# Performance work log

Hardware: AMD Instinct MI355X
Metric: run time of the kernel (lower is better)

The kernel has to match this reference:

```python
import jax, jax.numpy as jnp
import numpy as np

B, L, T = 256, 1024, 128

def setup_inputs() -> dict:
    key = jax.random.key(0)
    k1, k2, k3, k4 = jax.random.split(key, 4)
    inputs = jax.random.normal(k1, (B, L, T), dtype=jnp.float32)
    tag_indices = jax.random.randint(k2, (B, L), 0, T, dtype=jnp.int64)
    sequence_lengths = jax.random.randint(k3, (B,), 1, L + 1, dtype=jnp.int64)
    # xavier-ish scale for transitions
    transition_params = jax.random.normal(k4, (T, T), dtype=jnp.float32) * (2.0 / (T + T)) ** 0.5
    return {"inputs": inputs, "tag_indices": tag_indices,
            "sequence_lengths": sequence_lengths, "transition_params": transition_params}

def _crf_log_likelihood(inputs, tag_indices, sequence_lengths, transition_params):
    b, l, t = inputs.shape
    mask = (jnp.arange(l)[None, :] < sequence_lengths[:, None]).astype(inputs.dtype)  # [B,L]

    # --- unary score: sum_t inputs[b, t, tag[b,t]] over valid t ---
    unary = jnp.take_along_axis(inputs, tag_indices[:, :, None], axis=2)[:, :, 0]  # [B,L]
    unary_score = jnp.sum(unary * mask, axis=1)

    # --- binary score: sum_t trans[tag[t], tag[t+1]] masked by mask[:,1:] ---
    trans_sc = transition_params[tag_indices[:, :-1], tag_indices[:, 1:]]  # [B,L-1]
    binary_score = jnp.sum(trans_sc * mask[:, 1:], axis=1)
    sequence_scores = unary_score + binary_score

    # --- log normalizer via forward algorithm (log-space scan) ---
    first = inputs[:, 0]                               # [B,T]
    rest = jnp.transpose(inputs[:, 1:], (1, 0, 2))     # [L-1,B,T]

    def step(state, inp_t):
        # state: [B,T] previous alphas; transition broadcast: [B,T_prev,T_next]
        new = inp_t + jax.nn.logsumexp(state[:, :, None] + transition_params[None], axis=1)
        return new, new

    _, alphas = jax.lax.scan(step, first, rest)        # [L-1,B,T]
    # original indexes all_alphas at max(0, seq_len - 2)
    idx = jnp.clip(sequence_lengths - 2, 0, l - 2)
    final_alphas = alphas[idx, jnp.arange(b)]          # [B,T]
    log_norm = jax.nn.logsumexp(final_alphas, axis=1)
    log_norm = jnp.where(sequence_lengths <= 0, jnp.zeros_like(log_norm), log_norm)

    return sequence_scores - log_norm

def reference(inputs, tag_indices, sequence_lengths, transition_params):
    return _crf_log_likelihood(inputs, tag_indices, sequence_lengths, transition_params)
```

## Files before the change

kernel.cpp:

```cpp
#include <hip/hip_runtime.h>


#define B_   256
#define LL   1024
#define TT   128
#define NBLK 16
#define L2E  1.4426950408889634f
#define LN2f 0.6931471805599453f

typedef __attribute__((ext_vector_type(8))) short bf16x8;
typedef __attribute__((ext_vector_type(4))) float f32x4;
union bfrw { unsigned w[4]; bf16x8 v; };

__device__ __forceinline__ unsigned bfround(float x) {
    unsigned u = __float_as_uint(x);
    return u + 0x7fffu + ((u >> 16) & 1u);
}
__device__ __forceinline__ void lds_barrier() {
    asm volatile("s_waitcnt lgkmcnt(0)\n\ts_barrier" ::: "memory");
}

__global__ void crf_score(const float* __restrict__ inputs,
                          const int*   __restrict__ tags,
                          const int*   __restrict__ slens,
                          const float* __restrict__ trans,
                          float* __restrict__ scorebuf) {
    const int b = blockIdx.x, tid = threadIdx.x;
    const int lane = tid & 63, wid = tid >> 6;
    __shared__ float wsc[4];
    const int slen = slens[b];
    const float* inb  = inputs + (size_t)b * LL * TT;
    const int*   tagb = tags + b * LL;
    float sc = 0.f;
    for (int t = tid; t < slen; t += 256) {
        int tg = tagb[t];
        float v = inb[(size_t)t * TT + tg];
        if (t >= 1) v += trans[tagb[t - 1] * TT + tg];
        sc += v;
    }
    #pragma unroll
    for (int off = 32; off > 0; off >>= 1) sc += __shfl_xor(sc, off, 64);
    if (lane == 0) wsc[wid] = sc;
    __syncthreads();
    if (tid == 0) scorebuf[b] = wsc[0] + wsc[1] + wsc[2] + wsc[3];
}

template<bool FWD, int PH>
__device__ __forceinline__ void phase(int t, float& Dacc, float4 (&up)[4][2],
                                      const bf16x8 (&af)[2][4],
                                      short* qls, float* sb, const float* pu,
                                      float* __restrict__ qcap, float* __restrict__ rcap,
                                      float* __restrict__ dqv, float* __restrict__ drv,
                                      int cb, int tfin, int rank,
                                      int wid, int quad, int bl)
{
    constexpr int CUR  = PH & 1;
    constexpr int NXT  = CUR ^ 1;
    constexpr int SLOT = FWD ? ((1 + PH) & 3) : ((3 - PH) & 3);

    bfrw bfr[4];
    #pragma unroll
    for (int c = 0; c < 4; ++c)
        bfr[c].v = *(const bf16x8*)(qls + CUR * (16 * 136) + bl * 136 + (4 * c + quad) * 8);
    float sprev = sb[CUR * 16 + bl];

    float ex[8];
    #pragma unroll
    for (int mt = 0; mt < 2; ++mt) {
        float4 v = up[SLOT][mt];
        ex[4*mt+0] = __builtin_amdgcn_exp2f(v.x * L2E);
        ex[4*mt+1] = __builtin_amdgcn_exp2f(v.y * L2E);
        ex[4*mt+2] = __builtin_amdgcn_exp2f(v.z * L2E);
        ex[4*mt+3] = __builtin_amdgcn_exp2f(v.w * L2E);
    }
    {
        int tp = FWD ? (t + 4) : (t - 5);
        tp = tp < 0 ? 0 : (tp > LL - 1 ? LL - 1 : tp);
        #pragma unroll
        for (int mt = 0; mt < 2; ++mt)
            up[SLOT][mt] = *(const float4*)(pu + (size_t)tp * TT + mt * 16);
    }

    f32x4 a0 = {0.f,0.f,0.f,0.f}, a1 = {0.f,0.f,0.f,0.f};
    #pragma unroll
    for (int c = 0; c < 4; ++c) {
        a0 = __builtin_amdgcn_mfma_f32_16x16x32_bf16(af[0][c], bfr[c].v, a0, 0, 0, 0);
        a1 = __builtin_amdgcn_mfma_f32_16x16x32_bf16(af[1][c], bfr[c].v, a1, 0, 0, 0);
    }

    float ci = __builtin_amdgcn_rcpf(sprev);
    Dacc += __builtin_amdgcn_logf(sprev);
    float rv[8];
    #pragma unroll
    for (int r = 0; r < 4; ++r) { rv[r] = ci * a0[r]; rv[4 + r] = ci * a1[r]; }

    if (!FWD) {
        bool cap = (cb == t - 1);
        if (__any(cap)) {
            if (cap) {
                float4 s0 = {rv[0], rv[1], rv[2], rv[3]};
                float4 s1 = {rv[4], rv[5], rv[6], rv[7]};
                *(float4*)(rcap + rank * TT + wid * 32 + quad * 4) = s0;
                *(float4*)(rcap + rank * TT + wid * 32 + 16 + quad * 4) = s1;
                if (wid == 0 && quad == 0) drv[rank] = Dacc;
            }
        }
        bool inj = (tfin == t - 1);
        #pragma unroll
        for (int k = 0; k < 8; ++k) rv[k] = inj ? 1.0f : rv[k];
        Dacc = inj ? 0.0f : Dacc;
    }

    float ov[8];
    #pragma unroll
    for (int k = 0; k < 8; ++k) ov[k] = ex[k] * rv[k];

    if (FWD) {
        bool cap = (cb == t);
        if (__any(cap)) {
            if (cap) {
                float4 s0 = {ov[0], ov[1], ov[2], ov[3]};
                float4 s1 = {ov[4], ov[5], ov[6], ov[7]};
                *(float4*)(qcap + rank * TT + wid * 32 + quad * 4) = s0;
                *(float4*)(qcap + rank * TT + wid * 32 + 16 + quad * 4) = s1;
                if (wid == 0 && quad == 0) dqv[rank] = Dacc;
            }
        }
    }

    if (wid == 0 && quad == 0) sb[NXT * 16 + bl] = a0[0];

    bfrw pk;
    pk.w[0] = __builtin_amdgcn_perm(bfround(ov[1]), bfround(ov[0]), 0x07060302);
    pk.w[1] = __builtin_amdgcn_perm(bfround(ov[3]), bfround(ov[2]), 0x07060302);
    pk.w[2] = __builtin_amdgcn_perm(bfround(ov[5]), bfround(ov[4]), 0x07060302);
    pk.w[3] = __builtin_amdgcn_perm(bfround(ov[7]), bfround(ov[6]), 0x07060302);
    *(bf16x8*)(qls + NXT * (16 * 136) + bl * 136 + (4 * wid + quad) * 8) = pk.v;

    lds_barrier();
}

__launch_bounds__(256, 1)
__global__ void crf_scan(const float* __restrict__ inputs,
                         const int*   __restrict__ slens,
                         const float* __restrict__ trans,
                         float* __restrict__ qcap, float* __restrict__ rcap,
                         float* __restrict__ dqv,  float* __restrict__ drv,
                         int* __restrict__ perm)
{
    __shared__ __align__(16) short qls[2 * 16 * 136];
    __shared__ float sb[2 * 16];
    __shared__ int keys[B_];

    const int tid  = threadIdx.x;
    const int lane = tid & 63;
    const int wid  = __builtin_amdgcn_readfirstlane(tid >> 6);
    const int quad = lane >> 4;
    const int bl   = lane & 15;
    const bool isf = (blockIdx.x < NBLK);
    const int g    = isf ? blockIdx.x : blockIdx.x - NBLK;

    keys[tid] = slens[tid] * 256 + tid;
    __syncthreads();
    for (int k = 2; k <= B_; k <<= 1) {
        for (int s = k >> 1; s > 0; s >>= 1) {
            int ixj = tid ^ s;
            if (ixj > tid) {
                int a = keys[tid], b2 = keys[ixj];
                bool asc = ((tid & k) == 0);
                if ((a > b2) == asc) { keys[tid] = b2; keys[ixj] = a; }
            }
            __syncthreads();
        }
    }
    if (isf && tid < 16) perm[g * 16 + tid] = keys[g * 16 + tid] & 255;

    const int key = keys[g * 16 + bl];
    const int ob  = key & 255;
    const int sl  = key >> 8;
    int tfin = sl - 1; if (tfin < 1) tfin = 1;
    const int cb = tfin >> 1;

    int cmax = cb, cmin = cb, tmax = tfin;
    #pragma unroll
    for (int o = 1; o < 16; o <<= 1) {
        int a = __shfl_xor(cmax, o, 16); cmax = a > cmax ? a : cmax;
        int b2 = __shfl_xor(cmin, o, 16); cmin = b2 < cmin ? b2 : cmin;
        int c2 = __shfl_xor(tmax, o, 16); tmax = c2 > tmax ? c2 : tmax;
    }
    cmax = __builtin_amdgcn_readfirstlane(cmax);
    cmin = __builtin_amdgcn_readfirstlane(cmin);
    tmax = __builtin_amdgcn_readfirstlane(tmax);

    bf16x8 af[2][4];
    #pragma unroll
    for (int mt = 0; mt < 2; ++mt) {
        const int j = wid * 32 + mt * 16 + bl;
        #pragma unroll
        for (int c = 0; c < 4; ++c) {
            #pragma unroll
            for (int jj = 0; jj < 8; ++jj) {
                int k = 32 * c + 16 * (jj >> 2) + 4 * quad + (jj & 3);
                int idx = isf ? (k * TT + j) : (j * TT + k);
                float ev = __builtin_amdgcn_exp2f(trans[idx] * L2E);
                af[mt][c][jj] = (short)(bfround(ev) >> 16);
            }
        }
    }

    const float* pu = inputs + (size_t)ob * LL * TT + wid * 32 + quad * 4;
    const int rank = g * 16 + bl;
    float Dacc = 0.f;
    float4 up[4][2];

    if (tid < 16) sb[tid] = 1.0f;

    if (isf) {
        float q0[8];
        #pragma unroll
        for (int mt = 0; mt < 2; ++mt) {
            float4 v = *(const float4*)(pu + mt * 16);
            q0[4*mt+0] = __builtin_amdgcn_exp2f(v.x * L2E);
            q0[4*mt+1] = __builtin_amdgcn_exp2f(v.y * L2E);
            q0[4*mt+2] = __builtin_amdgcn_exp2f(v.z * L2E);
            q0[4*mt+3] = __builtin_amdgcn_exp2f(v.w * L2E);
        }
        bfrw pk;
        pk.w[0] = __builtin_amdgcn_perm(bfround(q0[1]), bfround(q0[0]), 0x07060302);
        pk.w[1] = __builtin_amdgcn_perm(bfround(q0[3]), bfround(q0[2]), 0x07060302);
        pk.w[2] = __builtin_amdgcn_perm(bfround(q0[5]), bfround(q0[4]), 0x07060302);
        pk.w[3] = __builtin_amdgcn_perm(bfround(q0[7]), bfround(q0[6]), 0x07060302);
        *(bf16x8*)(qls + bl * 136 + (4 * wid + quad) * 8) = pk.v;
        if (cb == 0) {
            float4 s0 = {q0[0], q0[1], q0[2], q0[3]};
            float4 s1 = {q0[4], q0[5], q0[6], q0[7]};
            *(float4*)(qcap + rank * TT + wid * 32 + quad * 4) = s0;
            *(float4*)(qcap + rank * TT + wid * 32 + 16 + quad * 4) = s1;
            if (wid == 0 && quad == 0) dqv[rank] = 0.f;
        }
        #pragma unroll
        for (int s = 1; s <= 4; ++s) {
            #pragma unroll
            for (int mt = 0; mt < 2; ++mt)
                up[s & 3][mt] = *(const float4*)(pu + (size_t)s * TT + mt * 16);
        }
        __syncthreads();

        for (int tb = 1; tb <= cmax; tb += 4) {
            phase<true,0>(tb+0, Dacc, up, af, qls, sb, pu, qcap, rcap, dqv, drv, cb, tfin, rank, wid, quad, bl);
            phase<true,1>(tb+1, Dacc, up, af, qls, sb, pu, qcap, rcap, dqv, drv, cb, tfin, rank, wid, quad, bl);
            phase<true,2>(tb+2, Dacc, up, af, qls, sb, pu, qcap, rcap, dqv, drv, cb, tfin, rank, wid, quad, bl);
            phase<true,3>(tb+3, Dacc, up, af, qls, sb, pu, qcap, rcap, dqv, drv, cb, tfin, rank, wid, quad, bl);
        }
    } else {
        bfrw pk;
        pk.w[0] = pk.w[1] = pk.w[2] = pk.w[3] = 0x3F803F80u;
        *(bf16x8*)(qls + bl * 136 + (4 * wid + quad) * 8) = pk.v;

        const int tb0 = (tmax + 4) & ~3;
        #pragma unroll
        for (int ph = 0; ph < 4; ++ph) {
            int ui = tb0 - 1 - ph;
            ui = ui > LL - 1 ? LL - 1 : (ui < 0 ? 0 : ui);
            #pragma unroll
            for (int mt = 0; mt < 2; ++mt)
                up[(3 - ph) & 3][mt] = *(const float4*)(pu + (size_t)ui * TT + mt * 16);
        }
        __syncthreads();

        for (int tb = tb0; tb > cmin; tb -= 4) {
            phase<false,0>(tb-0, Dacc, up, af, qls, sb, pu, qcap, rcap, dqv, drv, cb, tfin, rank, wid, quad, bl);
            phase<false,1>(tb-1, Dacc, up, af, qls, sb, pu, qcap, rcap, dqv, drv, cb, tfin, rank, wid, quad, bl);
            phase<false,2>(tb-2, Dacc, up, af, qls, sb, pu, qcap, rcap, dqv, drv, cb, tfin, rank, wid, quad, bl);
            phase<false,3>(tb-3, Dacc, up, af, qls, sb, pu, qcap, rcap, dqv, drv, cb, tfin, rank, wid, quad, bl);
        }
    }
}

__global__ void crf_comb(const float* __restrict__ qcap, const float* __restrict__ rcap,
                         const float* __restrict__ dqv, const float* __restrict__ drv,
                         const int* __restrict__ perm, const float* __restrict__ scorebuf,
                         float* __restrict__ out) {
    const int tid = threadIdx.x;
    const int r16 = tid >> 4, part = tid & 15;
    const int rank = blockIdx.x * 16 + r16;
    const float* qc = qcap + rank * TT + part * 8;
    const float* rc = rcap + rank * TT + part * 8;
    float4 a0 = *(const float4*)(qc);
    float4 a1 = *(const float4*)(qc + 4);
    float4 b0 = *(const float4*)(rc);
    float4 b1 = *(const float4*)(rc + 4);
    float s = a0.x*b0.x + a0.y*b0.y + a0.z*b0.z + a0.w*b0.w
            + a1.x*b1.x + a1.y*b1.y + a1.z*b1.z + a1.w*b1.w;
    #pragma unroll
    for (int o = 1; o < 16; o <<= 1) s += __shfl_xor(s, o, 16);
    if (part == 0) {
        int ob = perm[rank];
        float logZ = LN2f * (__builtin_amdgcn_logf(s) + dqv[rank] + drv[rank]);
        out[ob] = scorebuf[ob] - logZ;
    }
}

extern "C" void kernel_launch(void* const* d_in, const int* in_sizes, int n_in,
                              void* d_out, int out_size, void* d_ws, size_t ws_size,
                              hipStream_t stream) {
    const float* inputs = (const float*)d_in[0];
    const int*   tags   = (const int*)d_in[1];
    const int*   slens  = (const int*)d_in[2];
    const float* trans  = (const float*)d_in[3];
    float* out = (float*)d_out;

    float* qcap = (float*)d_ws;
    float* rcap = qcap + 32768;
    float* dqv  = rcap + 32768;
    float* drv  = dqv + 256;
    int*   perm = (int*)(drv + 256);
    float* scorebuf = (float*)(perm + 256);

    crf_score<<<B_, 256, 0, stream>>>(inputs, tags, slens, trans, scorebuf);
    crf_scan<<<2 * NBLK, 256, 0, stream>>>(inputs, slens, trans, qcap, rcap, dqv, drv, perm);
    crf_comb<<<NBLK, 256, 0, stream>>>(qcap, rcap, dqv, drv, perm, scorebuf, out);
}
```

Before: 430.7 us.

## Fuse score kernel into scan launch, rebalance meet-in-middle split, split MFMA chains

Moves the gold-path score computation into 64 extra blocks of the scan kernel, removing one launch and letting it run alongside the 32 scan blocks. The forward/backward meeting point becomes the group-wide midpoint of the longest sequence in each group rather than each sequence's own half, which balances the forward and backward blocks. The four chained MFMAs are split into two independent accumulator chains to shorten the dependency chain, and bf16 packing uses a hardware convert builtin when available. Risks: the extra blocks contend with the scan blocks for memory bandwidth, and the new capture logic for sequences whose meeting point equals their final step must stay correct.

```diff
diff --git a/kernel.cpp b/kernel.cpp
--- a/kernel.cpp
+++ b/kernel.cpp
@@ -16,33 +16,16 @@
     unsigned u = __float_as_uint(x);
     return u + 0x7fffu + ((u >> 16) & 1u);
 }
+__device__ __forceinline__ unsigned pack2(float lo, float hi) {
+#if __has_builtin(__builtin_amdgcn_cvt_pk_bf16_f32)
+    auto p = __builtin_amdgcn_cvt_pk_bf16_f32(lo, hi);
+    unsigned w; __builtin_memcpy(&w, &p, 4); return w;
+#else
+    return __builtin_amdgcn_perm(bfround(hi), bfround(lo), 0x07060302);
+#endif
+}
 __device__ __forceinline__ void lds_barrier() {
     asm volatile("s_waitcnt lgkmcnt(0)\n\ts_barrier" ::: "memory");
-}
-
-__global__ void crf_score(const float* __restrict__ inputs,
-                          const int*   __restrict__ tags,
-                          const int*   __restrict__ slens,
-                          const float* __restrict__ trans,
-                          float* __restrict__ scorebuf) {
-    const int b = blockIdx.x, tid = threadIdx.x;
-    const int lane = tid & 63, wid = tid >> 6;
-    __shared__ float wsc[4];
-    const int slen = slens[b];
-    const float* inb  = inputs + (size_t)b * LL * TT;
-    const int*   tagb = tags + b * LL;
-    float sc = 0.f;
-    for (int t = tid; t < slen; t += 256) {
-        int tg = tagb[t];
-        float v = inb[(size_t)t * TT + tg];
-        if (t >= 1) v += trans[tagb[t - 1] * TT + tg];
-        sc += v;
-    }
-    #pragma unroll
-    for (int off = 32; off > 0; off >>= 1) sc += __shfl_xor(sc, off, 64);
-    if (lane == 0) wsc[wid] = sc;
-    __syncthreads();
-    if (tid == 0) scorebuf[b] = wsc[0] + wsc[1] + wsc[2] + wsc[3];
 }
 
 template<bool FWD, int PH>
@@ -63,6 +46,18 @@
     for (int c = 0; c < 4; ++c)
         bfr[c].v = *(const bf16x8*)(qls + CUR * (16 * 136) + bl * 136 + (4 * c + quad) * 8);
     float sprev = sb[CUR * 16 + bl];
+    float ci = __builtin_amdgcn_rcpf(sprev);
+
+    f32x4 ae0 = {0.f,0.f,0.f,0.f}, ao0 = {0.f,0.f,0.f,0.f};
+    f32x4 ae1 = {0.f,0.f,0.f,0.f}, ao1 = {0.f,0.f,0.f,0.f};
+    ae0 = __builtin_amdgcn_mfma_f32_16x16x32_bf16(af[0][0], bfr[0].v, ae0, 0, 0, 0);
+    ae1 = __builtin_amdgcn_mfma_f32_16x16x32_bf16(af[1][0], bfr[0].v, ae1, 0, 0, 0);
+    ao0 = __builtin_amdgcn_mfma_f32_16x16x32_bf16(af[0][1], bfr[1].v, ao0, 0, 0, 0);
+    ao1 = __builtin_amdgcn_mfma_f32_16x16x32_bf16(af[1][1], bfr[1].v, ao1, 0, 0, 0);
+    ae0 = __builtin_amdgcn_mfma_f32_16x16x32_bf16(af[0][2], bfr[2].v, ae0, 0, 0, 0);
+    ae1 = __builtin_amdgcn_mfma_f32_16x16x32_bf16(af[1][2], bfr[2].v, ae1, 0, 0, 0);
+    ao0 = __builtin_amdgcn_mfma_f32_16x16x32_bf16(af[0][3], bfr[3].v, ao0, 0, 0, 0);
+    ao1 = __builtin_amdgcn_mfma_f32_16x16x32_bf16(af[1][3], bfr[3].v, ao1, 0, 0, 0);
 
     float ex[8];
     #pragma unroll
@@ -80,28 +75,23 @@
         for (int mt = 0; mt < 2; ++mt)
             up[SLOT][mt] = *(const float4*)(pu + (size_t)tp * TT + mt * 16);
     }
-
-    f32x4 a0 = {0.f,0.f,0.f,0.f}, a1 = {0.f,0.f,0.f,0.f};
-    #pragma unroll
-    for (int c = 0; c < 4; ++c) {
-        a0 = __builtin_amdgcn_mfma_f32_16x16x32_bf16(af[0][c], bfr[c].v, a0, 0, 0, 0);
-        a1 = __builtin_amdgcn_mfma_f32_16x16x32_bf16(af[1][c], bfr[c].v, a1, 0, 0, 0);
-    }
-
-    float ci = __builtin_amdgcn_rcpf(sprev);
     Dacc += __builtin_amdgcn_logf(sprev);
+
+    f32x4 s0v = ae0 + ao0;
+    f32x4 s1v = ae1 + ao1;
+
     float rv[8];
     #pragma unroll
-    for (int r = 0; r < 4; ++r) { rv[r] = ci * a0[r]; rv[4 + r] = ci * a1[r]; }
+    for (int r = 0; r < 4; ++r) { rv[r] = ci * s0v[r]; rv[4 + r] = ci * s1v[r]; }
 
     if (!FWD) {
-        bool cap = (cb == t - 1);
+        bool cap = (cb == t - 1) && (cb != tfin);
         if (__any(cap)) {
             if (cap) {
-                float4 s0 = {rv[0], rv[1], rv[2], rv[3]};
-                float4 s1 = {rv[4], rv[5], rv[6], rv[7]};
-                *(float4*)(rcap + rank * TT + wid * 32 + quad * 4) = s0;
-                *(float4*)(rcap + rank * TT + wid * 32 + 16 + quad * 4) = s1;
+                float4 c0 = {rv[0], rv[1], rv[2], rv[3]};
+                float4 c1 = {rv[4], rv[5], rv[6], rv[7]};
+                *(float4*)(rcap + rank * TT + wid * 32 + quad * 4) = c0;
+                *(float4*)(rcap + rank * TT + wid * 32 + 16 + quad * 4) = c1;
                 if (wid == 0 && quad == 0) drv[rank] = Dacc;
             }
         }
@@ -119,22 +109,22 @@
         bool cap = (cb == t);
         if (__any(cap)) {
             if (cap) {
-                float4 s0 = {ov[0], ov[1], ov[2], ov[3]};
-                float4 s1 = {ov[4], ov[5], ov[6], ov[7]};
-                *(float4*)(qcap + rank * TT + wid * 32 + quad * 4) = s0;
-                *(float4*)(qcap + rank * TT + wid * 32 + 16 + quad * 4) = s1;
+                float4 c0 = {ov[0], ov[1], ov[2], ov[3]};
+                float4 c1 = {ov[4], ov[5], ov[6], ov[7]};
+                *(float4*)(qcap + rank * TT + wid * 32 + quad * 4) = c0;
+                *(float4*)(qcap + rank * TT + wid * 32 + 16 + quad * 4) = c1;
                 if (wid == 0 && quad == 0) dqv[rank] = Dacc;
             }
         }
     }
 
-    if (wid == 0 && quad == 0) sb[NXT * 16 + bl] = a0[0];
+    if (wid == 0 && quad == 0) sb[NXT * 16 + bl] = s0v[0];
 
     bfrw pk;
-    pk.w[0] = __builtin_amdgcn_perm(bfround(ov[1]), bfround(ov[0]), 0x07060302);
-    pk.w[1] = __builtin_amdgcn_perm(bfround(ov[3]), bfround(ov[2]), 0x07060302);
-    pk.w[2] = __builtin_amdgcn_perm(bfround(ov[5]), bfround(ov[4]), 0x07060302);
-    pk.w[3] = __builtin_amdgcn_perm(bfround(ov[7]), bfround(ov[6]), 0x07060302);
+    pk.w[0] = pack2(ov[0], ov[1]);
+    pk.w[1] = pack2(ov[2], ov[3]);
+    pk.w[2] = pack2(ov[4], ov[5]);
+    pk.w[3] = pack2(ov[6], ov[7]);
     *(bf16x8*)(qls + NXT * (16 * 136) + bl * 136 + (4 * wid + quad) * 8) = pk.v;
 
     lds_barrier();
@@ -142,17 +132,45 @@
 
 __launch_bounds__(256, 1)
 __global__ void crf_scan(const float* __restrict__ inputs,
+                         const int*   __restrict__ tags,
                          const int*   __restrict__ slens,
                          const float* __restrict__ trans,
                          float* __restrict__ qcap, float* __restrict__ rcap,
                          float* __restrict__ dqv,  float* __restrict__ drv,
-                         int* __restrict__ perm)
+                         int* __restrict__ perm, float* __restrict__ scorebuf)
 {
     __shared__ __align__(16) short qls[2 * 16 * 136];
     __shared__ float sb[2 * 16];
     __shared__ int keys[B_];
 
     const int tid  = threadIdx.x;
+
+    if (blockIdx.x >= 2 * NBLK) {
+        const int sbid = blockIdx.x - 2 * NBLK;
+        const int lane = tid & 63, wid = tid >> 6;
+        #pragma unroll 1
+        for (int bi = 0; bi < 4; ++bi) {
+            const int b = sbid * 4 + bi;
+            const int slen = slens[b];
+            const float* inb  = inputs + (size_t)b * LL * TT;
+            const int*   tagb = tags + b * LL;
+            float sc = 0.f;
+            for (int t = tid; t < slen; t += 256) {
+                int tg = tagb[t];
+                float v = inb[(size_t)t * TT + tg];
+                if (t >= 1) v += trans[tagb[t - 1] * TT + tg];
+                sc += v;
+            }
+            #pragma unroll
+            for (int off = 32; off > 0; off >>= 1) sc += __shfl_xor(sc, off, 64);
+            if (lane == 0) sb[wid] = sc;
+            __syncthreads();
+            if (tid == 0) scorebuf[b] = sb[0] + sb[1] + sb[2] + sb[3];
+            __syncthreads();
+        }
+        return;
+    }
+
     const int lane = tid & 63;
     const int wid  = __builtin_amdgcn_readfirstlane(tid >> 6);
     const int quad = lane >> 4;
@@ -179,18 +197,25 @@
     const int ob  = key & 255;
     const int sl  = key >> 8;
     int tfin = sl - 1; if (tfin < 1) tfin = 1;
-    const int cb = tfin >> 1;
-
-    int cmax = cb, cmin = cb, tmax = tfin;
+
+    int tmax = tfin;
+    #pragma unroll
+    for (int o = 1; o < 16; o <<= 1) {
+        int c2 = __shfl_xor(tmax, o, 16); tmax = c2 > tmax ? c2 : tmax;
+    }
+    tmax = __builtin_amdgcn_readfirstlane(tmax);
+
+    const int C  = (tmax + 4) >> 1;
+    const int cb = tfin < C ? tfin : C;
+
+    int cmax = cb, cmin = cb;
     #pragma unroll
     for (int o = 1; o < 16; o <<= 1) {
         int a = __shfl_xor(cmax, o, 16); cmax = a > cmax ? a : cmax;
         int b2 = __shfl_xor(cmin, o, 16); cmin = b2 < cmin ? b2 : cmin;
-        int c2 = __shfl_xor(tmax, o, 16); tmax = c2 > tmax ? c2 : tmax;
     }
     cmax = __builtin_amdgcn_readfirstlane(cmax);
     cmin = __builtin_amdgcn_readfirstlane(cmin);
-    tmax = __builtin_amdgcn_readfirstlane(tmax);
 
     bf16x8 af[2][4];
     #pragma unroll
@@ -226,18 +251,12 @@
             q0[4*mt+3] = __builtin_amdgcn_exp2f(v.w * L2E);
         }
         bfrw pk;
-        pk.w[0] = __builtin_amdgcn_perm(bfround(q0[1]), bfround(q0[0]), 0x07060302);
-        pk.w[1] = __builtin_amdgcn_perm(bfround(q0[3]), bfround(q0[2]), 0x07060302);
-        pk.w[2] = __builtin_amdgcn_perm(bfround(q0[5]), bfround(q0[4]), 0x07060302);
-        pk.w[3] = __builtin_amdgcn_perm(bfround(q0[7]), bfround(q0[6]), 0x07060302);
+        pk.w[0] = pack2(q0[0], q0[1]);
+        pk.w[1] = pack2(q0[2], q0[3]);
+        pk.w[2] = pack2(q0[4], q0[5]);
+        pk.w[3] = pack2(q0[6], q0[7]);
         *(bf16x8*)(qls + bl * 136 + (4 * wid + quad) * 8) = pk.v;
-        if (cb == 0) {
-            float4 s0 = {q0[0], q0[1], q0[2], q0[3]};
-            float4 s1 = {q0[4], q0[5], q0[6], q0[7]};
-            *(float4*)(qcap + rank * TT + wid * 32 + quad * 4) = s0;
-            *(float4*)(qcap + rank * TT + wid * 32 + 16 + quad * 4) = s1;
-            if (wid == 0 && quad == 0) dqv[rank] = 0.f;
-        }
+
         #pragma unroll
         for (int s = 1; s <= 4; ++s) {
             #pragma unroll
@@ -256,6 +275,12 @@
         bfrw pk;
         pk.w[0] = pk.w[1] = pk.w[2] = pk.w[3] = 0x3F803F80u;
         *(bf16x8*)(qls + bl * 136 + (4 * wid + quad) * 8) = pk.v;
+        if (cb == tfin) {
+            float4 one4 = {1.f, 1.f, 1.f, 1.f};
+            *(float4*)(rcap + rank * TT + wid * 32 + quad * 4) = one4;
+            *(float4*)(rcap + rank * TT + wid * 32 + 16 + quad * 4) = one4;
+            if (wid == 0 && quad == 0) drv[rank] = 0.f;
+        }
 
         const int tb0 = (tmax + 4) & ~3;
         #pragma unroll
@@ -317,7 +342,7 @@
     int*   perm = (int*)(drv + 256);
     float* scorebuf = (float*)(perm + 256);
 
-    crf_score<<<B_, 256, 0, stream>>>(inputs, tags, slens, trans, scorebuf);
-    crf_scan<<<2 * NBLK, 256, 0, stream>>>(inputs, slens, trans, qcap, rcap, dqv, drv, perm);
+    crf_scan<<<2 * NBLK + 64, 256, 0, stream>>>(inputs, tags, slens, trans,
+                                                qcap, rcap, dqv, drv, perm, scorebuf);
     crf_comb<<<NBLK, 256, 0, stream>>>(qcap, rcap, dqv, drv, perm, scorebuf, out);
 }
```

Measured after the change: 412.5 us. 1.04x faster.
